# Kernel optimization log

Hardware: AMD Instinct MI355X
Metric: run time of the kernel (lower is better)

The kernel has to match this reference:

```python
import jax, jax.numpy as jnp
import numpy as np

D_MODEL = 1024
N_HEADS = 16
D_FF = 4096
D_K = D_MODEL // N_HEADS


def _ln(x, g, b, eps=1e-5):
    mu = jnp.mean(x, axis=-1, keepdims=True)
    var = jnp.mean(jnp.square(x - mu), axis=-1, keepdims=True)
    return (x - mu) * jax.lax.rsqrt(var + eps) * g + b


def setup_inputs() -> dict:
    key = jax.random.key(0)
    ks = jax.random.split(key, 16)
    s = 0.02
    inp = {
        "x": jax.random.normal(ks[0], (2, 2048, D_MODEL), dtype=jnp.float32),
        "Wq": jax.random.normal(ks[1], (D_MODEL, D_MODEL), dtype=jnp.float32) * s,
        "bq": jnp.zeros((D_MODEL,), jnp.float32),
        "Wk": jax.random.normal(ks[2], (D_MODEL, D_MODEL), dtype=jnp.float32) * s,
        "bk": jnp.zeros((D_MODEL,), jnp.float32),
        "Wv": jax.random.normal(ks[3], (D_MODEL, D_MODEL), dtype=jnp.float32) * s,
        "bv": jnp.zeros((D_MODEL,), jnp.float32),
        "Wo": jax.random.normal(ks[4], (D_MODEL, D_MODEL), dtype=jnp.float32) * s,
        "bo": jnp.zeros((D_MODEL,), jnp.float32),
        "W1": jax.random.normal(ks[5], (D_MODEL, D_FF), dtype=jnp.float32) * s,
        "b1": jnp.zeros((D_FF,), jnp.float32),
        "W2": jax.random.normal(ks[6], (D_FF, D_MODEL), dtype=jnp.float32) * s,
        "b2": jnp.zeros((D_MODEL,), jnp.float32),
        "g1": jnp.ones((D_MODEL,), jnp.float32),
        "be1": jnp.zeros((D_MODEL,), jnp.float32),
        "g2": jnp.ones((D_MODEL,), jnp.float32),
        "be2": jnp.zeros((D_MODEL,), jnp.float32),
    }
    return inp


def reference(x, Wq, bq, Wk, bk, Wv, bv, Wo, bo, W1, b1, W2, b2, g1, be1, g2, be2):
    B, L, D = x.shape
    # QKV projections -> [B, H, L, d_k]
    q = (x @ Wq + bq).reshape(B, L, N_HEADS, D_K).transpose(0, 2, 1, 3)
    k = (x @ Wk + bk).reshape(B, L, N_HEADS, D_K).transpose(0, 2, 1, 3)
    v = (x @ Wv + bv).reshape(B, L, N_HEADS, D_K).transpose(0, 2, 1, 3)
    scores = jnp.einsum("bhqd,bhkd->bhqk", q, k) / jnp.sqrt(jnp.float32(D_K))
    attn = jax.nn.softmax(scores, axis=-1)
    ctx = jnp.einsum("bhqk,bhkd->bhqd", attn, v)
    ctx = ctx.transpose(0, 2, 1, 3).reshape(B, L, D)
    attn_out = ctx @ Wo + bo
    # residual + LN1
    h = _ln(x + attn_out, g1, be1)
    # FFN (exact GELU, matching torch F.gelu default)
    ff = jax.nn.gelu(h @ W1 + b1, approximate=False) @ W2 + b2
    return _ln(h + ff, g2, be2)
```

## Files before the change

### kernel.cpp

```cpp
#include <hip/hip_runtime.h>
#include <cmath>


typedef unsigned short u16;
typedef unsigned int u32;
typedef __attribute__((ext_vector_type(8))) __bf16 bf16x8;
typedef __attribute__((ext_vector_type(4))) float f32x4;

#define MFMA16(a, b, c) __builtin_amdgcn_mfma_f32_16x16x32_bf16(a, b, c, 0, 0, 0)

__device__ __forceinline__ u16 f2bf(float f) {
  u32 u = __builtin_bit_cast(u32, f);
  u += 0x7fffu + ((u >> 16) & 1u);
  return (u16)(u >> 16);
}

__device__ __forceinline__ u32 packtrunc(float lo, float hi) {
#if __has_builtin(__builtin_amdgcn_perm)
  return __builtin_amdgcn_perm(__builtin_bit_cast(u32, hi),
                               __builtin_bit_cast(u32, lo), 0x07060302u);
#else
  return (__builtin_bit_cast(u32, lo) >> 16) |
         (__builtin_bit_cast(u32, hi) & 0xFFFF0000u);
#endif
}

__device__ __forceinline__ bf16x8 ld_frag(const u16* p) {
  return __builtin_bit_cast(bf16x8, *(const uint4*)p);
}

__device__ __forceinline__ float fexp2(float x) {
#if __has_builtin(__builtin_amdgcn_exp2f)
  return __builtin_amdgcn_exp2f(x);
#else
  return exp2f(x);
#endif
}

__device__ __forceinline__ void gload16(const u16* g, u16* l) {
  __builtin_amdgcn_global_load_lds(
      (const __attribute__((address_space(1))) void*)g,
      (__attribute__((address_space(3))) void*)l, 16, 0, 0);
}

#define WAITVL(N) asm volatile("s_waitcnt vmcnt(" #N ") lgkmcnt(0)" ::: "memory")
#define BAR() do { __builtin_amdgcn_s_barrier(); asm volatile("" ::: "memory"); } while (0)

__global__ __launch_bounds__(256) void cvt_bf16_k(const float* __restrict__ src,
                                                  u16* __restrict__ dst) {
  int i = (blockIdx.x * 256 + threadIdx.x) * 4;
  float4 v = *(const float4*)(src + i);
  ushort4 o;
  o.x = f2bf(v.x); o.y = f2bf(v.y); o.z = f2bf(v.z); o.w = f2bf(v.w);
  *(ushort4*)(dst + i) = o;
}

__global__ __launch_bounds__(256) void transpose_bf16_k(const float* __restrict__ src,
                                                        u16* __restrict__ dst,
                                                        int R, int C) {
  __shared__ float tile[32][33];
  int tx = threadIdx.x & 31, ty = threadIdx.x >> 5;
  int c0 = blockIdx.x * 32, r0 = blockIdx.y * 32;
#pragma unroll
  for (int i = 0; i < 4; i++)
    tile[ty + 8 * i][tx] = src[(long)(r0 + ty + 8 * i) * C + c0 + tx];
  __syncthreads();
#pragma unroll
  for (int i = 0; i < 4; i++)
    dst[(long)(c0 + ty + 8 * i) * R + r0 + tx] = f2bf(tile[tx][ty + 8 * i]);
}

__global__ __launch_bounds__(256) void transpose4_bf16_k(
    const float* __restrict__ Wq, const float* __restrict__ Wk,
    const float* __restrict__ Wv, const float* __restrict__ Wo,
    u16* __restrict__ wqkvT, u16* __restrict__ woT) {
  const int z = blockIdx.z;
  const float* src = (z == 0) ? Wq : (z == 1) ? Wk : (z == 2) ? Wv : Wo;
  u16* dst = (z < 3) ? (wqkvT + (size_t)z * 1024 * 1024) : woT;
  __shared__ float tile[32][33];
  int tx = threadIdx.x & 31, ty = threadIdx.x >> 5;
  int c0 = blockIdx.x * 32, r0 = blockIdx.y * 32;
#pragma unroll
  for (int i = 0; i < 4; i++)
    tile[ty + 8 * i][tx] = src[(long)(r0 + ty + 8 * i) * 1024 + c0 + tx];
  __syncthreads();
#pragma unroll
  for (int i = 0; i < 4; i++)
    dst[(long)(c0 + ty + 8 * i) * 1024 + r0 + tx] = f2bf(tile[tx][ty + 8 * i]);
}

template <int MODE>
__global__ __launch_bounds__(512, 2) void gemm256_k(
    const u16* __restrict__ A, const u16* __restrict__ BT,
    int N, int lda, int ldb, int Kc,
    const float* __restrict__ bias, float* __restrict__ outF, u16* __restrict__ outB,
    float* __restrict__ p1, float* __restrict__ p2, float* __restrict__ p3,
    u16* __restrict__ qd, u16* __restrict__ kd, u16* __restrict__ vTd,
    const float* __restrict__ bq, const float* __restrict__ bk, const float* __restrict__ bv) {
  __shared__ u16 As[4][256 * 32];
  __shared__ u16 Bs[4][256 * 32];
  const int tid = threadIdx.x;
  const int wave = tid >> 6, lane = tid & 63, quad = lane >> 4, l16 = lane & 15;
  const int wm = wave >> 2, wn = wave & 3;
  const int m0 = blockIdx.y * 256, n0 = blockIdx.x * 256;
  const int kz = blockIdx.z;
  const long kofs = (long)kz * Kc;
  const int KT = Kc >> 5;

  const int srow = lane >> 2;
  const int sseg = (lane & 3) ^ (srow & 3);
  const u16* aS = A + (long)(m0 + wave * 32 + srow) * lda + kofs + sseg * 8;
  const u16* bS = BT + (long)(n0 + wave * 32 + srow) * ldb + kofs + sseg * 8;

  auto stageA = [&](int sb, int s) {
    const u16* p = aS + (long)s * 32;
    gload16(p, &As[sb][wave * 1024]);
    gload16(p + 16 * (long)lda, &As[sb][wave * 1024 + 512]);
  };
  auto stageB = [&](int sb, int s) {
    const u16* p = bS + (long)s * 32;
    gload16(p, &Bs[sb][wave * 1024]);
    gload16(p + 16 * (long)ldb, &Bs[sb][wave * 1024 + 512]);
  };

  int aro[8], bro[4];
#pragma unroll
  for (int mf = 0; mf < 8; mf++) {
    int r = wm * 128 + mf * 16 + l16;
    aro[mf] = r * 32 + ((quad ^ (r & 3)) * 8);
  }
#pragma unroll
  for (int nf = 0; nf < 4; nf++) {
    int r = wn * 64 + nf * 16 + l16;
    bro[nf] = r * 32 + ((quad ^ (r & 3)) * 8);
  }

  f32x4 acc[8][4] = {};

  stageA(0, 0); stageB(0, 0);
  stageA(1, 1); stageB(1, 1);
  stageA(2, 2); stageB(2, 2);

#pragma unroll 1
  for (int t = 0; t < KT; ++t) {
    const int buf = t & 3;
    if (t < KT - 2)      { WAITVL(8); }
    else if (t == KT - 2){ WAITVL(4); }
    else                 { WAITVL(0); }
    BAR();

    if (t + 3 < KT) stageA((t + 3) & 3, t + 3);
    bf16x8 af[4], bf4[4];
#pragma unroll
    for (int i = 0; i < 4; i++) af[i] = ld_frag(&As[buf][aro[i]]);
#pragma unroll
    for (int i = 0; i < 4; i++) bf4[i] = ld_frag(&Bs[buf][bro[i]]);
    __builtin_amdgcn_s_setprio(1);
#pragma unroll
    for (int mf = 0; mf < 4; mf++)
#pragma unroll
      for (int nf = 0; nf < 4; nf++)
        acc[mf][nf] = MFMA16(af[mf], bf4[nf], acc[mf][nf]);
    __builtin_amdgcn_s_setprio(0);

    if (t + 3 < KT) stageB((t + 3) & 3, t + 3);
#pragma unroll
    for (int i = 0; i < 4; i++) af[i] = ld_frag(&As[buf][aro[4 + i]]);
    __builtin_amdgcn_s_setprio(1);
#pragma unroll
    for (int mf = 0; mf < 4; mf++)
#pragma unroll
      for (int nf = 0; nf < 4; nf++)
        acc[4 + mf][nf] = MFMA16(af[mf], bf4[nf], acc[4 + mf][nf]);
    __builtin_amdgcn_s_setprio(0);
  }

  if (MODE == 0) {
    const int nbase = n0 + wn * 64;
    const int mat = nbase >> 10;
    const float* bp = (mat == 0) ? bq : ((mat == 1) ? bk : bv);
    float bb[4];
    int hh0[4], dd0[4];
#pragma unroll
    for (int nf = 0; nf < 4; nf++) {
      int nn = (nbase + nf * 16 + l16) & 1023;
      bb[nf] = bp[nn];
      hh0[nf] = nn >> 6;
      dd0[nf] = nn & 63;
    }
    if (mat < 2) {
#pragma unroll
      for (int mf = 0; mf < 8; mf++) {
#pragma unroll
        for (int r = 0; r < 4; r++) {
          int mr = m0 + wm * 128 + mf * 16 + quad * 4 + r;
          int bI = mr >> 11, ll = mr & 2047;
#pragma unroll
          for (int nf = 0; nf < 4; nf++) {
            float v = acc[mf][nf][r] + bb[nf];
            long idx = ((long)((bI * 16 + hh0[nf]) * 2048 + ll)) * 64 + dd0[nf];
            if (mat == 0) {
              qd[idx] = f2bf(v * 0.18033688011112043f);
            } else {
              kd[idx] = f2bf(v);
            }
          }
        }
      }
    } else {
#pragma unroll
      for (int nf = 0; nf < 4; nf++) {
#pragma unroll
        for (int mf = 0; mf < 8; mf++) {
#pragma unroll
          for (int r = 0; r < 4; r++) {
            int mr = m0 + wm * 128 + mf * 16 + quad * 4 + r;
            int bI = mr >> 11, ll = mr & 2047;
            float v = acc[mf][nf][r] + bb[nf];
            vTd[((long)((bI * 16 + hh0[nf]) * 64 + dd0[nf])) * 2048 + ll] = f2bf(v);
          }
        }
      }
    }
  } else if (MODE == 2) {
    float bb[4];
#pragma unroll
    for (int nf = 0; nf < 4; nf++) bb[nf] = bias[n0 + wn * 64 + nf * 16 + l16];
#pragma unroll
    for (int mf = 0; mf < 8; mf++) {
#pragma unroll
      for (int r = 0; r < 4; r++) {
        int mr = m0 + wm * 128 + mf * 16 + quad * 4 + r;
        u16* orow = outB + (long)mr * N + n0 + wn * 64 + l16;
#pragma unroll
        for (int nf = 0; nf < 4; nf++) {
          float v = acc[mf][nf][r] + bb[nf];
          v = 0.5f * v * (1.0f + erff(v * 0.70710678118654752f));
          orow[nf * 16] = f2bf(v);
        }
      }
    }
  } else {
    float* sl = (kz == 0) ? outF : (kz == 1) ? p1 : (kz == 2) ? p2 : p3;
#pragma unroll
    for (int mf = 0; mf < 8; mf++) {
#pragma unroll
      for (int r = 0; r < 4; r++) {
        int mr = m0 + wm * 128 + mf * 16 + quad * 4 + r;
        float* orow = sl + (long)mr * N + n0 + wn * 64 + l16;
#pragma unroll
        for (int nf = 0; nf < 4; nf++) orow[nf * 16] = acc[mf][nf][r];
      }
    }
  }
}

template <int MODE, int TN>
__global__ __launch_bounds__(256) void gemm_k(
    const u16* __restrict__ A, const u16* __restrict__ BT, int M, int N, int K,
    const float* __restrict__ bias, float* __restrict__ outF, u16* __restrict__ outB,
    u16* __restrict__ qd, u16* __restrict__ kd, u16* __restrict__ vTd,
    const float* __restrict__ bq, const float* __restrict__ bk, const float* __restrict__ bv) {
  constexpr int NT = TN / 32;
  __shared__ u16 As[2][128 * 32];
  __shared__ u16 Bs[2][TN * 32];
  const int tid = threadIdx.x;
  const int wave = tid >> 6, lane = tid & 63, quad = lane >> 4, l16 = lane & 15;
  const int wm = wave >> 1, wn = wave & 1;
  const int m0 = blockIdx.y * 128, n0 = blockIdx.x * TN;

  const int srow = lane >> 2;
  const int sxor = (lane & 3) ^ (srow & 3);
  const u16* aS0 = A + (long)(m0 + wave * 32 + srow) * K + sxor * 8;
  const u16* aS1 = aS0 + 16 * K;
  const u16* bS0 = BT + (long)(n0 + (TN == 128 ? wave * 32 : wave * 16) + srow) * K + sxor * 8;
  const u16* bS1 = bS0 + 16 * K;

  int aoff[4], boff[NT];
#pragma unroll
  for (int t = 0; t < 4; t++) {
    int ra = wm * 64 + t * 16 + l16;
    aoff[t] = ra * 32 + ((quad ^ (l16 & 3)) * 8);
  }
#pragma unroll
  for (int t = 0; t < NT; t++) {
    int rb = wn * (TN / 2) + t * 16 + l16;
    boff[t] = rb * 32 + ((quad ^ (l16 & 3)) * 8);
  }

  auto stage = [&](int buf, int k0) {
    gload16(aS0 + k0, &As[buf][(wave * 2 + 0) * 512]);
    gload16(aS1 + k0, &As[buf][(wave * 2 + 1) * 512]);
    if (TN == 128) {
      gload16(bS0 + k0, &Bs[buf][(wave * 2 + 0) * 512]);
      gload16(bS1 + k0, &Bs[buf][(wave * 2 + 1) * 512]);
    } else {
      gload16(bS0 + k0, &Bs[buf][wave * 512]);
    }
  };

  f32x4 acc[4][NT] = {};

  stage(0, 0);
#pragma unroll 1
  for (int k0 = 0; k0 < K; k0 += 32) {
    const int buf = (k0 >> 5) & 1;
    __syncthreads();
    if (k0 + 32 < K) stage(buf ^ 1, k0 + 32);
    bf16x8 af[4], bfr[NT];
#pragma unroll
    for (int t = 0; t < 4; t++) af[t] = ld_frag(&As[buf][aoff[t]]);
#pragma unroll
    for (int t = 0; t < NT; t++) bfr[t] = ld_frag(&Bs[buf][boff[t]]);
#pragma unroll
    for (int mt = 0; mt < 4; mt++)
#pragma unroll
      for (int nt = 0; nt < NT; nt++)
        acc[mt][nt] = MFMA16(af[mt], bfr[nt], acc[mt][nt]);
  }

  if (MODE == 1) {
    float bb[NT];
#pragma unroll
    for (int nt = 0; nt < NT; nt++) bb[nt] = bias[n0 + wn * (TN / 2) + nt * 16 + l16];
#pragma unroll
    for (int mt = 0; mt < 4; mt++) {
#pragma unroll
      for (int r = 0; r < 4; r++) {
        int mr = m0 + wm * 64 + mt * 16 + quad * 4 + r;
        float* orow = outF + (long)mr * N + n0 + wn * (TN / 2) + l16;
#pragma unroll
        for (int nt = 0; nt < NT; nt++)
          orow[nt * 16] = acc[mt][nt][r] + bb[nt];
      }
    }
  }
}

__global__ __launch_bounds__(256) void attn_k(const u16* __restrict__ qd,
                                              const u16* __restrict__ kd,
                                              const u16* __restrict__ vTd,
                                              u16* __restrict__ ctx) {
  __shared__ u16 Ks[2][64 * 64];
  __shared__ u16 Vs[2][64 * 64];
  __shared__ __align__(16) u16 P[4][32][72];
  const int tid = threadIdx.x;
  const int wave = tid >> 6, lane = tid & 63, quad = lane >> 4, l16 = lane & 15;
  const int bh = blockIdx.y;
  const u16* Q = qd + (long)bh * 2048 * 64;
  const u16* Kp = kd + (long)bh * 2048 * 64;
  const u16* Vt = vTd + (long)bh * 64 * 2048;
  const int qbase = blockIdx.x * 128 + wave * 32;

  bf16x8 qf[2][2];
#pragma unroll
  for (int qs = 0; qs < 2; qs++) {
    qf[qs][0] = ld_frag(Q + (qbase + qs * 16 + l16) * 64 + quad * 8);
    qf[qs][1] = ld_frag(Q + (qbase + qs * 16 + l16) * 64 + 32 + quad * 8);
  }

  f32x4 o[2][4] = {};
  float m[2] = {-1e30f, -1e30f}, l[2] = {0.f, 0.f};

  const int srow = lane >> 3;
  const int sx = (lane & 7) ^ srow;
  const int kr0 = wave * 16 + srow;
  const int kr1 = wave * 16 + 8 + srow;

  const int fs0 = ((0 * 4 + quad) ^ (l16 & 7)) * 8;
  const int fs1 = ((1 * 4 + quad) ^ (l16 & 7)) * 8;

  auto stage = [&](int buf, int j0) {
    gload16(Kp + (long)(j0 + kr0) * 64 + sx * 8, &Ks[buf][(wave * 2 + 0) * 512]);
    gload16(Kp + (long)(j0 + kr1) * 64 + sx * 8, &Ks[buf][(wave * 2 + 1) * 512]);
    gload16(Vt + (long)kr0 * 2048 + j0 + sx * 8, &Vs[buf][(wave * 2 + 0) * 512]);
    gload16(Vt + (long)kr1 * 2048 + j0 + sx * 8, &Vs[buf][(wave * 2 + 1) * 512]);
  };

  stage(0, 0);

#pragma unroll 1
  for (int j0 = 0; j0 < 2048; j0 += 64) {
    const int buf = (j0 >> 6) & 1;
    __syncthreads();
    if (j0 + 64 < 2048) stage(buf ^ 1, j0 + 64);

    const u16* kb = &Ks[buf][0];
    f32x4 st[2][4];
#pragma unroll
    for (int f = 0; f < 4; f++) {
      bf16x8 k0 = ld_frag(kb + (f * 16 + l16) * 64 + fs0);
      bf16x8 k1 = ld_frag(kb + (f * 16 + l16) * 64 + fs1);
      f32x4 s0 = {}, s1 = {};
      s0 = MFMA16(k0, qf[0][0], s0); s0 = MFMA16(k1, qf[0][1], s0);
      s1 = MFMA16(k0, qf[1][0], s1); s1 = MFMA16(k1, qf[1][1], s1);
      st[0][f] = s0; st[1][f] = s1;
    }

#pragma unroll
    for (int qs = 0; qs < 2; qs++) {
      float mx = -1e30f;
#pragma unroll
      for (int f = 0; f < 4; f++)
        mx = fmaxf(mx, fmaxf(fmaxf(st[qs][f][0], st[qs][f][1]),
                             fmaxf(st[qs][f][2], st[qs][f][3])));
      mx = fmaxf(mx, __shfl_xor(mx, 16));
      mx = fmaxf(mx, __shfl_xor(mx, 32));
      if (__ballot(mx > m[qs])) {
        float mn = fmaxf(m[qs], mx);
        float al = fexp2(m[qs] - mn);
        m[qs] = mn;
        l[qs] *= al;
#pragma unroll
        for (int nt = 0; nt < 4; nt++) {
          o[qs][nt][0] *= al; o[qs][nt][1] *= al;
          o[qs][nt][2] *= al; o[qs][nt][3] *= al;
        }
      }
      float sm = 0.f;
      u16* prow = &P[wave][qs * 16 + l16][0];
#pragma unroll
      for (int f = 0; f < 4; f++) {
        float p0 = fexp2(st[qs][f][0] - m[qs]);
        float p1 = fexp2(st[qs][f][1] - m[qs]);
        float p2 = fexp2(st[qs][f][2] - m[qs]);
        float p3 = fexp2(st[qs][f][3] - m[qs]);
        sm += (p0 + p1) + (p2 + p3);
        uint2 u;
        u.x = packtrunc(p0, p1);
        u.y = packtrunc(p2, p3);
        *(uint2*)(prow + f * 16 + quad * 4) = u;
      }
      sm += __shfl_xor(sm, 16);
      sm += __shfl_xor(sm, 32);
      l[qs] += sm;
    }
    __asm__ volatile("s_waitcnt lgkmcnt(0)" ::: "memory");

    const u16* vb = &Vs[buf][0];
    bf16x8 vf[4][2];
#pragma unroll
    for (int nt = 0; nt < 4; nt++) {
      vf[nt][0] = ld_frag(vb + (nt * 16 + l16) * 64 + fs0);
      vf[nt][1] = ld_frag(vb + (nt * 16 + l16) * 64 + fs1);
    }
#pragma unroll
    for (int qs = 0; qs < 2; qs++) {
      const u16* prow = &P[wave][qs * 16 + l16][0];
#pragma unroll
      for (int kh = 0; kh < 2; kh++) {
        bf16x8 pf = ld_frag(prow + kh * 32 + quad * 8);
#pragma unroll
        for (int nt = 0; nt < 4; nt++)
          o[qs][nt] = MFMA16(vf[nt][kh], pf, o[qs][nt]);
      }
    }
  }

  const int bI = bh >> 4, hh = bh & 15;
#pragma unroll
  for (int qs = 0; qs < 2; qs++) {
    const float rl = 1.0f / l[qs];
    const long row = (long)(bI * 2048 + qbase + qs * 16 + l16);
#pragma unroll
    for (int nt = 0; nt < 4; nt++) {
      ushort4 w;
      w.x = f2bf(o[qs][nt][0] * rl);
      w.y = f2bf(o[qs][nt][1] * rl);
      w.z = f2bf(o[qs][nt][2] * rl);
      w.w = f2bf(o[qs][nt][3] * rl);
      *(ushort4*)(ctx + row * 1024 + hh * 64 + nt * 16 + quad * 4) = w;
    }
  }
}

__global__ __launch_bounds__(256) void ln_k(const float* __restrict__ a,
                                            const float* __restrict__ b,
                                            const float* __restrict__ g,
                                            const float* __restrict__ be,
                                            float* __restrict__ outF,
                                            u16* __restrict__ outB) {
  const int row = blockIdx.x, tid = threadIdx.x;
  const float* pa = a + (long)row * 1024;
  const float* pb = b + (long)row * 1024;
  float v[4], s = 0.f, sq = 0.f;
#pragma unroll
  for (int i = 0; i < 4; i++) {
    int c = i * 256 + tid;
    v[i] = pa[c] + pb[c];
    s += v[i];
    sq += v[i] * v[i];
  }
#pragma unroll
  for (int off = 1; off < 64; off <<= 1) {
    s += __shfl_xor(s, off);
    sq += __shfl_xor(sq, off);
  }
  __shared__ float red[10];
  int wave = tid >> 6, lane = tid & 63;
  if (lane == 0) { red[wave * 2] = s; red[wave * 2 + 1] = sq; }
  __syncthreads();
  if (tid == 0) {
    float S = red[0] + red[2] + red[4] + red[6];
    float Q = red[1] + red[3] + red[5] + red[7];
    float mu = S * (1.0f / 1024.0f);
    float var = Q * (1.0f / 1024.0f) - mu * mu;
    red[8] = mu;
    red[9] = rsqrtf(var + 1e-5f);
  }
  __syncthreads();
  float mu = red[8], rstd = red[9];
#pragma unroll
  for (int i = 0; i < 4; i++) {
    int c = i * 256 + tid;
    float o = (v[i] - mu) * rstd * g[c] + be[c];
    outF[(long)row * 1024 + c] = o;
    if (outB) outB[(long)row * 1024 + c] = f2bf(o);
  }
}

__global__ __launch_bounds__(256) void ln4_k(const float* __restrict__ a,
                                             const float* __restrict__ q0,
                                             const float* __restrict__ q1,
                                             const float* __restrict__ q2,
                                             const float* __restrict__ q3,
                                             const float* __restrict__ bias,
                                             const float* __restrict__ g,
                                             const float* __restrict__ be,
                                             float* __restrict__ outF) {
  const int row = blockIdx.x, tid = threadIdx.x;
  const long base = (long)row * 1024;
  float v[4], s = 0.f, sq = 0.f;
#pragma unroll
  for (int i = 0; i < 4; i++) {
    int c = i * 256 + tid;
    float ff = (q0[base + c] + q1[base + c]) + (q2[base + c] + q3[base + c]) + bias[c];
    v[i] = a[base + c] + ff;
    s += v[i];
    sq += v[i] * v[i];
  }
#pragma unroll
  for (int off = 1; off < 64; off <<= 1) {
    s += __shfl_xor(s, off);
    sq += __shfl_xor(sq, off);
  }
  __shared__ float red[10];
  int wave = tid >> 6, lane = tid & 63;
  if (lane == 0) { red[wave * 2] = s; red[wave * 2 + 1] = sq; }
  __syncthreads();
  if (tid == 0) {
    float S = red[0] + red[2] + red[4] + red[6];
    float Q = red[1] + red[3] + red[5] + red[7];
    float mu = S * (1.0f / 1024.0f);
    float var = Q * (1.0f / 1024.0f) - mu * mu;
    red[8] = mu;
    red[9] = rsqrtf(var + 1e-5f);
  }
  __syncthreads();
  float mu = red[8], rstd = red[9];
#pragma unroll
  for (int i = 0; i < 4; i++) {
    int c = i * 256 + tid;
    outF[base + c] = (v[i] - mu) * rstd * g[c] + be[c];
  }
}

extern "C" void kernel_launch(void* const* d_in, const int* in_sizes, int n_in,
                              void* d_out, int out_size, void* d_ws, size_t ws_size,
                              hipStream_t stream) {
  const float* x  = (const float*)d_in[0];
  const float* Wq = (const float*)d_in[1];  const float* bq = (const float*)d_in[2];
  const float* Wk = (const float*)d_in[3];  const float* bk = (const float*)d_in[4];
  const float* Wv = (const float*)d_in[5];  const float* bv = (const float*)d_in[6];
  const float* Wo = (const float*)d_in[7];  const float* bo = (const float*)d_in[8];
  const float* W1 = (const float*)d_in[9];  const float* b1 = (const float*)d_in[10];
  const float* W2 = (const float*)d_in[11]; const float* b2 = (const float*)d_in[12];
  const float* g1 = (const float*)d_in[13]; const float* be1 = (const float*)d_in[14];
  const float* g2 = (const float*)d_in[15]; const float* be2 = (const float*)d_in[16];

  char* ws = (char*)d_ws;
  size_t off = 0;
  auto alloc = [&](size_t bytes) {
    size_t o = off;
    off += (bytes + 255) & ~(size_t)255;
    return o;
  };
  u16*   xb     = (u16*)(ws + alloc(4096UL * 1024 * 2));
  u16*   wqkvT  = (u16*)(ws + alloc(3072UL * 1024 * 2));
  u16*   woT    = (u16*)(ws + alloc(1024UL * 1024 * 2));
  u16*   w1T    = (u16*)(ws + alloc(4096UL * 1024 * 2));
  u16*   w2T    = (u16*)(ws + alloc(1024UL * 4096 * 2));
  u16*   qb     = (u16*)(ws + alloc(32UL * 2048 * 64 * 2));
  u16*   kb     = (u16*)(ws + alloc(32UL * 2048 * 64 * 2));
  u16*   vTb    = (u16*)(ws + alloc(32UL * 64 * 2048 * 2));
  u16*   ctx    = (u16*)(ws + alloc(4096UL * 1024 * 2));
  float* attnO  = (float*)(ws + alloc(4096UL * 1024 * 4));
  float* h      = (float*)(ws + alloc(4096UL * 1024 * 4));
  u16*   hb     = (u16*)(ws + alloc(4096UL * 1024 * 2));
  u16*   ff1    = (u16*)(ws + alloc(4096UL * 4096 * 2));
  float* ff2    = (float*)(ws + alloc(4096UL * 1024 * 4));
  if (off > ws_size) return;

  float* sl0 = ff2;
  float* sl1 = attnO;
  float* sl2 = (float*)qb;
  float* sl3 = (float*)vTb;

  cvt_bf16_k<<<4096, 256, 0, stream>>>(x, xb);
  transpose4_bf16_k<<<dim3(32, 32, 4), 256, 0, stream>>>(Wq, Wk, Wv, Wo, wqkvT, woT);
  transpose_bf16_k<<<dim3(128, 32), 256, 0, stream>>>(W1, w1T, 1024, 4096);
  transpose_bf16_k<<<dim3(32, 128), 256, 0, stream>>>(W2, w2T, 4096, 1024);

  gemm256_k<0><<<dim3(12, 16), 512, 0, stream>>>(
      xb, wqkvT, 3072, 1024, 1024, 1024,
      nullptr, nullptr, nullptr, nullptr, nullptr, nullptr,
      qb, kb, vTb, bq, bk, bv);
  attn_k<<<dim3(16, 32), 256, 0, stream>>>(qb, kb, vTb, ctx);
  gemm_k<1, 64><<<dim3(16, 32), 256, 0, stream>>>(ctx, woT, 4096, 1024, 1024,
                                                  bo, attnO, nullptr,
                                                  nullptr, nullptr, nullptr, nullptr, nullptr, nullptr);
  ln_k<<<4096, 256, 0, stream>>>(x, attnO, g1, be1, h, hb);
  gemm256_k<2><<<dim3(16, 16), 512, 0, stream>>>(
      hb, w1T, 4096, 1024, 1024, 1024,
      b1, nullptr, ff1, nullptr, nullptr, nullptr,
      nullptr, nullptr, nullptr, nullptr, nullptr, nullptr);
  gemm256_k<3><<<dim3(4, 16, 4), 512, 0, stream>>>(
      ff1, w2T, 1024, 4096, 4096, 1024,
      nullptr, sl0, nullptr, sl1, sl2, sl3,
      nullptr, nullptr, nullptr, nullptr, nullptr, nullptr);
  ln4_k<<<4096, 256, 0, stream>>>(h, sl0, sl1, sl2, sl3, b2, g2, be2, (float*)d_out);
}
```

Measured before the change: 411.5 us.

## Split attention over key halves with combine kernel; add barriers in GEMM loop

Attention is split along the key dimension into two halves (flash-decoding style). This doubles the grid from 512 to 1024 blocks so more CUs are occupied, and a new combine kernel merges the partial outputs using the per-row max and sum. The online softmax now rescales only when the running max grows by more than 8, which skips rescale work but lets exponent values grow (up to 2^8) before renormalising. Separately, the 256 GEMM loop now loads fragments before issuing the next stage and adds extra barriers, which changes how LDS reads interleave with global prefetch at the cost of more synchronisation. The partial results go to fp32 scratch buffers reused from other workspace, adding global traffic.

```diff
diff --git a/kernel.cpp b/kernel.cpp
--- a/kernel.cpp
+++ b/kernel.cpp
@@ -149,12 +149,13 @@
     else                 { WAITVL(0); }
     BAR();
 
+    bf16x8 af[4], bf4[4];
+#pragma unroll
+    for (int i = 0; i < 4; i++) af[i] = ld_frag(&As[buf][aro[i]]);
+#pragma unroll
+    for (int i = 0; i < 4; i++) bf4[i] = ld_frag(&Bs[buf][bro[i]]);
     if (t + 3 < KT) stageA((t + 3) & 3, t + 3);
-    bf16x8 af[4], bf4[4];
-#pragma unroll
-    for (int i = 0; i < 4; i++) af[i] = ld_frag(&As[buf][aro[i]]);
-#pragma unroll
-    for (int i = 0; i < 4; i++) bf4[i] = ld_frag(&Bs[buf][bro[i]]);
+    BAR();
     __builtin_amdgcn_s_setprio(1);
 #pragma unroll
     for (int mf = 0; mf < 4; mf++)
@@ -163,15 +164,17 @@
         acc[mf][nf] = MFMA16(af[mf], bf4[nf], acc[mf][nf]);
     __builtin_amdgcn_s_setprio(0);
 
+    bf16x8 ag[4];
+#pragma unroll
+    for (int i = 0; i < 4; i++) ag[i] = ld_frag(&As[buf][aro[4 + i]]);
     if (t + 3 < KT) stageB((t + 3) & 3, t + 3);
-#pragma unroll
-    for (int i = 0; i < 4; i++) af[i] = ld_frag(&As[buf][aro[4 + i]]);
+    BAR();
     __builtin_amdgcn_s_setprio(1);
 #pragma unroll
     for (int mf = 0; mf < 4; mf++)
 #pragma unroll
       for (int nf = 0; nf < 4; nf++)
-        acc[4 + mf][nf] = MFMA16(af[mf], bf4[nf], acc[4 + mf][nf]);
+        acc[4 + mf][nf] = MFMA16(ag[mf], bf4[nf], acc[4 + mf][nf]);
     __builtin_amdgcn_s_setprio(0);
   }
 
@@ -340,13 +343,18 @@
 __global__ __launch_bounds__(256) void attn_k(const u16* __restrict__ qd,
                                               const u16* __restrict__ kd,
                                               const u16* __restrict__ vTd,
-                                              u16* __restrict__ ctx) {
+                                              float* __restrict__ oP0,
+                                              float* __restrict__ oP1,
+                                              float* __restrict__ ml0,
+                                              float* __restrict__ ml1) {
   __shared__ u16 Ks[2][64 * 64];
   __shared__ u16 Vs[2][64 * 64];
   __shared__ __align__(16) u16 P[4][32][72];
   const int tid = threadIdx.x;
   const int wave = tid >> 6, lane = tid & 63, quad = lane >> 4, l16 = lane & 15;
   const int bh = blockIdx.y;
+  const int kz = blockIdx.z;
+  const int jbeg = kz * 1024, jend = jbeg + 1024;
   const u16* Q = qd + (long)bh * 2048 * 64;
   const u16* Kp = kd + (long)bh * 2048 * 64;
   const u16* Vt = vTd + (long)bh * 64 * 2048;
@@ -377,13 +385,13 @@
     gload16(Vt + (long)kr1 * 2048 + j0 + sx * 8, &Vs[buf][(wave * 2 + 1) * 512]);
   };
 
-  stage(0, 0);
+  stage(0, jbeg);
 
 #pragma unroll 1
-  for (int j0 = 0; j0 < 2048; j0 += 64) {
+  for (int j0 = jbeg; j0 < jend; j0 += 64) {
     const int buf = (j0 >> 6) & 1;
     __syncthreads();
-    if (j0 + 64 < 2048) stage(buf ^ 1, j0 + 64);
+    if (j0 + 64 < jend) stage(buf ^ 1, j0 + 64);
 
     const u16* kb = &Ks[buf][0];
     f32x4 st[2][4];
@@ -406,7 +414,7 @@
                              fmaxf(st[qs][f][2], st[qs][f][3])));
       mx = fmaxf(mx, __shfl_xor(mx, 16));
       mx = fmaxf(mx, __shfl_xor(mx, 32));
-      if (__ballot(mx > m[qs])) {
+      if (__any(mx > m[qs] + 8.0f)) {
         float mn = fmaxf(m[qs], mx);
         float al = fexp2(m[qs] - mn);
         m[qs] = mn;
@@ -457,21 +465,44 @@
     }
   }
 
-  const int bI = bh >> 4, hh = bh & 15;
+  float* oDst = kz ? oP1 : oP0;
+  float* mlDst = kz ? ml1 : ml0;
 #pragma unroll
   for (int qs = 0; qs < 2; qs++) {
-    const float rl = 1.0f / l[qs];
-    const long row = (long)(bI * 2048 + qbase + qs * 16 + l16);
-#pragma unroll
-    for (int nt = 0; nt < 4; nt++) {
-      ushort4 w;
-      w.x = f2bf(o[qs][nt][0] * rl);
-      w.y = f2bf(o[qs][nt][1] * rl);
-      w.z = f2bf(o[qs][nt][2] * rl);
-      w.w = f2bf(o[qs][nt][3] * rl);
-      *(ushort4*)(ctx + row * 1024 + hh * 64 + nt * 16 + quad * 4) = w;
-    }
-  }
+    const long row = (long)bh * 2048 + qbase + qs * 16 + l16;
+#pragma unroll
+    for (int nt = 0; nt < 4; nt++)
+      *(float4*)(oDst + row * 64 + nt * 16 + quad * 4) =
+          *(const float4*)&o[qs][nt];
+    if (quad == 0) {
+      float2 ml2 = {m[qs], l[qs]};
+      *(float2*)(mlDst + row * 2) = ml2;
+    }
+  }
+}
+
+__global__ __launch_bounds__(256) void attn_combine_k(
+    const float* __restrict__ o0, const float* __restrict__ o1,
+    const float* __restrict__ ml0, const float* __restrict__ ml1,
+    u16* __restrict__ ctx) {
+  long i = ((long)blockIdx.x * 256 + threadIdx.x) * 4;
+  long row = i >> 6;
+  int d = (int)(i & 63);
+  float2 a0 = *(const float2*)(ml0 + row * 2);
+  float2 a1 = *(const float2*)(ml1 + row * 2);
+  float M = fmaxf(a0.x, a1.x);
+  float w0 = fexp2(a0.x - M), w1 = fexp2(a1.x - M);
+  float rinv = 1.0f / (a0.y * w0 + a1.y * w1);
+  float4 v0 = *(const float4*)(o0 + i);
+  float4 v1 = *(const float4*)(o1 + i);
+  int bh = (int)(row >> 11), ll = (int)(row & 2047);
+  int bI = bh >> 4, hh = bh & 15;
+  ushort4 w;
+  w.x = f2bf((v0.x * w0 + v1.x * w1) * rinv);
+  w.y = f2bf((v0.y * w0 + v1.y * w1) * rinv);
+  w.z = f2bf((v0.z * w0 + v1.z * w1) * rinv);
+  w.w = f2bf((v0.w * w0 + v1.w * w1) * rinv);
+  *(ushort4*)(ctx + ((long)(bI * 2048 + ll) * 1024) + hh * 64 + d) = w;
 }
 
 __global__ __launch_bounds__(256) void ln_k(const float* __restrict__ a,
@@ -601,6 +632,11 @@
   float* ff2    = (float*)(ws + alloc(4096UL * 1024 * 4));
   if (off > ws_size) return;
 
+  float* oPart0 = attnO;
+  float* oPart1 = h;
+  float* mlP0   = (float*)hb;
+  float* mlP1   = (float*)hb + 32 * 2048 * 2;
+
   float* sl0 = ff2;
   float* sl1 = attnO;
   float* sl2 = (float*)qb;
@@ -615,7 +651,9 @@
       xb, wqkvT, 3072, 1024, 1024, 1024,
       nullptr, nullptr, nullptr, nullptr, nullptr, nullptr,
       qb, kb, vTb, bq, bk, bv);
-  attn_k<<<dim3(16, 32), 256, 0, stream>>>(qb, kb, vTb, ctx);
+  attn_k<<<dim3(16, 32, 2), 256, 0, stream>>>(qb, kb, vTb,
+                                              oPart0, oPart1, mlP0, mlP1);
+  attn_combine_k<<<4096, 256, 0, stream>>>(oPart0, oPart1, mlP0, mlP1, ctx);
   gemm_k<1, 64><<<dim3(16, 32), 256, 0, stream>>>(ctx, woT, 4096, 1024, 1024,
                                                   bo, attnO, nullptr,
                                                   nullptr, nullptr, nullptr, nullptr, nullptr, nullptr);
```

New measurement: 399.0 us. -3.0%, faster.

## Switch big GEMMs to 128x128 tiles, halve split-K, and lazily rescale attention

Applied to the files above, without the earlier changes.

Replaces the 256x256, 512-thread GEMM, which used a 4-stage LDS pipeline, with a 128x128, 256-thread GEMM that uses a 3-stage pipeline and allows three blocks per CU. The goal is to launch more blocks, so the QKV, FFN1 and FFN2 grids fill the CUs better. FFN2 split-K drops from 4 to 2 slices, so the final layernorm sums two partials instead of four. Attention now rescales the running softmax only when the new max exceeds the old one by more than 8, and attn_k gets launch bounds for occupancy. The trade-off is less data reuse per tile, which means more global and LDS traffic for each FLOP.

```diff
diff --git a/kernel.cpp b/kernel.cpp
--- a/kernel.cpp
+++ b/kernel.cpp
@@ -90,19 +90,20 @@
 }
 
 template <int MODE>
-__global__ __launch_bounds__(512, 2) void gemm256_k(
+__global__ __launch_bounds__(256, 3) void gemm128_k(
     const u16* __restrict__ A, const u16* __restrict__ BT,
     int N, int lda, int ldb, int Kc,
-    const float* __restrict__ bias, float* __restrict__ outF, u16* __restrict__ outB,
-    float* __restrict__ p1, float* __restrict__ p2, float* __restrict__ p3,
+    const float* __restrict__ bias, float* __restrict__ outF,
+    u16* __restrict__ outB, float* __restrict__ p1,
     u16* __restrict__ qd, u16* __restrict__ kd, u16* __restrict__ vTd,
-    const float* __restrict__ bq, const float* __restrict__ bk, const float* __restrict__ bv) {
-  __shared__ u16 As[4][256 * 32];
-  __shared__ u16 Bs[4][256 * 32];
+    const float* __restrict__ bq, const float* __restrict__ bk,
+    const float* __restrict__ bv) {
+  __shared__ u16 As[3][128 * 32];
+  __shared__ u16 Bs[3][128 * 32];
   const int tid = threadIdx.x;
   const int wave = tid >> 6, lane = tid & 63, quad = lane >> 4, l16 = lane & 15;
-  const int wm = wave >> 2, wn = wave & 3;
-  const int m0 = blockIdx.y * 256, n0 = blockIdx.x * 256;
+  const int wm = wave >> 1, wn = wave & 1;
+  const int m0 = blockIdx.y * 128, n0 = blockIdx.x * 128;
   const int kz = blockIdx.z;
   const long kofs = (long)kz * Kc;
   const int KT = Kc >> 5;
@@ -112,67 +113,50 @@
   const u16* aS = A + (long)(m0 + wave * 32 + srow) * lda + kofs + sseg * 8;
   const u16* bS = BT + (long)(n0 + wave * 32 + srow) * ldb + kofs + sseg * 8;
 
-  auto stageA = [&](int sb, int s) {
-    const u16* p = aS + (long)s * 32;
-    gload16(p, &As[sb][wave * 1024]);
-    gload16(p + 16 * (long)lda, &As[sb][wave * 1024 + 512]);
+  auto stage = [&](int sb, int s) {
+    const u16* pa = aS + (long)s * 32;
+    gload16(pa, &As[sb][wave * 1024]);
+    gload16(pa + 16 * (long)lda, &As[sb][wave * 1024 + 512]);
+    const u16* pb = bS + (long)s * 32;
+    gload16(pb, &Bs[sb][wave * 1024]);
+    gload16(pb + 16 * (long)ldb, &Bs[sb][wave * 1024 + 512]);
   };
-  auto stageB = [&](int sb, int s) {
-    const u16* p = bS + (long)s * 32;
-    gload16(p, &Bs[sb][wave * 1024]);
-    gload16(p + 16 * (long)ldb, &Bs[sb][wave * 1024 + 512]);
-  };
-
-  int aro[8], bro[4];
-#pragma unroll
-  for (int mf = 0; mf < 8; mf++) {
-    int r = wm * 128 + mf * 16 + l16;
-    aro[mf] = r * 32 + ((quad ^ (r & 3)) * 8);
-  }
-#pragma unroll
-  for (int nf = 0; nf < 4; nf++) {
-    int r = wn * 64 + nf * 16 + l16;
-    bro[nf] = r * 32 + ((quad ^ (r & 3)) * 8);
-  }
-
-  f32x4 acc[8][4] = {};
-
-  stageA(0, 0); stageB(0, 0);
-  stageA(1, 1); stageB(1, 1);
-  stageA(2, 2); stageB(2, 2);
-
+
+  int aro[4], bro[4];
+#pragma unroll
+  for (int f = 0; f < 4; f++) {
+    int ra = wm * 64 + f * 16 + l16;
+    aro[f] = ra * 32 + ((quad ^ (ra & 3)) * 8);
+    int rb = wn * 64 + f * 16 + l16;
+    bro[f] = rb * 32 + ((quad ^ (rb & 3)) * 8);
+  }
+
+  f32x4 acc[4][4] = {};
+
+  stage(0, 0);
+  stage(1, 1);
+  int buf = 0;
 #pragma unroll 1
   for (int t = 0; t < KT; ++t) {
-    const int buf = t & 3;
-    if (t < KT - 2)      { WAITVL(8); }
-    else if (t == KT - 2){ WAITVL(4); }
-    else                 { WAITVL(0); }
+    if (t < KT - 1) { WAITVL(4); } else { WAITVL(0); }
     BAR();
-
-    if (t + 3 < KT) stageA((t + 3) & 3, t + 3);
-    bf16x8 af[4], bf4[4];
+    bf16x8 af[4], bfr[4];
 #pragma unroll
     for (int i = 0; i < 4; i++) af[i] = ld_frag(&As[buf][aro[i]]);
 #pragma unroll
-    for (int i = 0; i < 4; i++) bf4[i] = ld_frag(&Bs[buf][bro[i]]);
+    for (int i = 0; i < 4; i++) bfr[i] = ld_frag(&Bs[buf][bro[i]]);
+    if (t + 2 < KT) {
+      int nb = buf + 2; if (nb >= 3) nb -= 3;
+      stage(nb, t + 2);
+    }
     __builtin_amdgcn_s_setprio(1);
 #pragma unroll
     for (int mf = 0; mf < 4; mf++)
 #pragma unroll
       for (int nf = 0; nf < 4; nf++)
-        acc[mf][nf] = MFMA16(af[mf], bf4[nf], acc[mf][nf]);
+        acc[mf][nf] = MFMA16(af[mf], bfr[nf], acc[mf][nf]);
     __builtin_amdgcn_s_setprio(0);
-
-    if (t + 3 < KT) stageB((t + 3) & 3, t + 3);
-#pragma unroll
-    for (int i = 0; i < 4; i++) af[i] = ld_frag(&As[buf][aro[4 + i]]);
-    __builtin_amdgcn_s_setprio(1);
-#pragma unroll
-    for (int mf = 0; mf < 4; mf++)
-#pragma unroll
-      for (int nf = 0; nf < 4; nf++)
-        acc[4 + mf][nf] = MFMA16(af[mf], bf4[nf], acc[4 + mf][nf]);
-    __builtin_amdgcn_s_setprio(0);
+    if (++buf == 3) buf = 0;
   }
 
   if (MODE == 0) {
@@ -190,10 +174,10 @@
     }
     if (mat < 2) {
 #pragma unroll
-      for (int mf = 0; mf < 8; mf++) {
+      for (int mf = 0; mf < 4; mf++) {
 #pragma unroll
         for (int r = 0; r < 4; r++) {
-          int mr = m0 + wm * 128 + mf * 16 + quad * 4 + r;
+          int mr = m0 + wm * 64 + mf * 16 + quad * 4 + r;
           int bI = mr >> 11, ll = mr & 2047;
 #pragma unroll
           for (int nf = 0; nf < 4; nf++) {
@@ -211,10 +195,10 @@
 #pragma unroll
       for (int nf = 0; nf < 4; nf++) {
 #pragma unroll
-        for (int mf = 0; mf < 8; mf++) {
+        for (int mf = 0; mf < 4; mf++) {
 #pragma unroll
           for (int r = 0; r < 4; r++) {
-            int mr = m0 + wm * 128 + mf * 16 + quad * 4 + r;
+            int mr = m0 + wm * 64 + mf * 16 + quad * 4 + r;
             int bI = mr >> 11, ll = mr & 2047;
             float v = acc[mf][nf][r] + bb[nf];
             vTd[((long)((bI * 16 + hh0[nf]) * 64 + dd0[nf])) * 2048 + ll] = f2bf(v);
@@ -227,10 +211,10 @@
 #pragma unroll
     for (int nf = 0; nf < 4; nf++) bb[nf] = bias[n0 + wn * 64 + nf * 16 + l16];
 #pragma unroll
-    for (int mf = 0; mf < 8; mf++) {
+    for (int mf = 0; mf < 4; mf++) {
 #pragma unroll
       for (int r = 0; r < 4; r++) {
-        int mr = m0 + wm * 128 + mf * 16 + quad * 4 + r;
+        int mr = m0 + wm * 64 + mf * 16 + quad * 4 + r;
         u16* orow = outB + (long)mr * N + n0 + wn * 64 + l16;
 #pragma unroll
         for (int nf = 0; nf < 4; nf++) {
@@ -241,12 +225,12 @@
       }
     }
   } else {
-    float* sl = (kz == 0) ? outF : (kz == 1) ? p1 : (kz == 2) ? p2 : p3;
-#pragma unroll
-    for (int mf = 0; mf < 8; mf++) {
+    float* sl = (kz == 0) ? outF : p1;
+#pragma unroll
+    for (int mf = 0; mf < 4; mf++) {
 #pragma unroll
       for (int r = 0; r < 4; r++) {
-        int mr = m0 + wm * 128 + mf * 16 + quad * 4 + r;
+        int mr = m0 + wm * 64 + mf * 16 + quad * 4 + r;
         float* orow = sl + (long)mr * N + n0 + wn * 64 + l16;
 #pragma unroll
         for (int nf = 0; nf < 4; nf++) orow[nf * 16] = acc[mf][nf][r];
@@ -258,9 +242,7 @@
 template <int MODE, int TN>
 __global__ __launch_bounds__(256) void gemm_k(
     const u16* __restrict__ A, const u16* __restrict__ BT, int M, int N, int K,
-    const float* __restrict__ bias, float* __restrict__ outF, u16* __restrict__ outB,
-    u16* __restrict__ qd, u16* __restrict__ kd, u16* __restrict__ vTd,
-    const float* __restrict__ bq, const float* __restrict__ bk, const float* __restrict__ bv) {
+    const float* __restrict__ bias, float* __restrict__ outF) {
   constexpr int NT = TN / 32;
   __shared__ u16 As[2][128 * 32];
   __shared__ u16 Bs[2][TN * 32];
@@ -337,10 +319,10 @@
   }
 }
 
-__global__ __launch_bounds__(256) void attn_k(const u16* __restrict__ qd,
-                                              const u16* __restrict__ kd,
-                                              const u16* __restrict__ vTd,
-                                              u16* __restrict__ ctx) {
+__global__ __launch_bounds__(256, 3) void attn_k(const u16* __restrict__ qd,
+                                                 const u16* __restrict__ kd,
+                                                 const u16* __restrict__ vTd,
+                                                 u16* __restrict__ ctx) {
   __shared__ u16 Ks[2][64 * 64];
   __shared__ u16 Vs[2][64 * 64];
   __shared__ __align__(16) u16 P[4][32][72];
@@ -406,7 +388,7 @@
                              fmaxf(st[qs][f][2], st[qs][f][3])));
       mx = fmaxf(mx, __shfl_xor(mx, 16));
       mx = fmaxf(mx, __shfl_xor(mx, 32));
-      if (__ballot(mx > m[qs])) {
+      if (__any(mx > m[qs] + 8.0f)) {
         float mn = fmaxf(m[qs], mx);
         float al = fexp2(m[qs] - mn);
         m[qs] = mn;
@@ -519,22 +501,20 @@
   }
 }
 
-__global__ __launch_bounds__(256) void ln4_k(const float* __restrict__ a,
-                                             const float* __restrict__ q0,
-                                             const float* __restrict__ q1,
-                                             const float* __restrict__ q2,
-                                             const float* __restrict__ q3,
-                                             const float* __restrict__ bias,
-                                             const float* __restrict__ g,
-                                             const float* __restrict__ be,
-                                             float* __restrict__ outF) {
+__global__ __launch_bounds__(256) void ln2s_k(const float* __restrict__ a,
+                                              const float* __restrict__ q0,
+                                              const float* __restrict__ q1,
+                                              const float* __restrict__ bias,
+                                              const float* __restrict__ g,
+                                              const float* __restrict__ be,
+                                              float* __restrict__ outF) {
   const int row = blockIdx.x, tid = threadIdx.x;
   const long base = (long)row * 1024;
   float v[4], s = 0.f, sq = 0.f;
 #pragma unroll
   for (int i = 0; i < 4; i++) {
     int c = i * 256 + tid;
-    float ff = (q0[base + c] + q1[base + c]) + (q2[base + c] + q3[base + c]) + bias[c];
+    float ff = q0[base + c] + q1[base + c] + bias[c];
     v[i] = a[base + c] + ff;
     s += v[i];
     sq += v[i] * v[i];
@@ -603,30 +583,27 @@
 
   float* sl0 = ff2;
   float* sl1 = attnO;
-  float* sl2 = (float*)qb;
-  float* sl3 = (float*)vTb;
 
   cvt_bf16_k<<<4096, 256, 0, stream>>>(x, xb);
   transpose4_bf16_k<<<dim3(32, 32, 4), 256, 0, stream>>>(Wq, Wk, Wv, Wo, wqkvT, woT);
   transpose_bf16_k<<<dim3(128, 32), 256, 0, stream>>>(W1, w1T, 1024, 4096);
   transpose_bf16_k<<<dim3(32, 128), 256, 0, stream>>>(W2, w2T, 4096, 1024);
 
-  gemm256_k<0><<<dim3(12, 16), 512, 0, stream>>>(
+  gemm128_k<0><<<dim3(24, 32), 256, 0, stream>>>(
       xb, wqkvT, 3072, 1024, 1024, 1024,
-      nullptr, nullptr, nullptr, nullptr, nullptr, nullptr,
+      nullptr, nullptr, nullptr, nullptr,
       qb, kb, vTb, bq, bk, bv);
   attn_k<<<dim3(16, 32), 256, 0, stream>>>(qb, kb, vTb, ctx);
   gemm_k<1, 64><<<dim3(16, 32), 256, 0, stream>>>(ctx, woT, 4096, 1024, 1024,
-                                                  bo, attnO, nullptr,
-                                                  nullptr, nullptr, nullptr, nullptr, nullptr, nullptr);
+                                                  bo, attnO);
   ln_k<<<4096, 256, 0, stream>>>(x, attnO, g1, be1, h, hb);
-  gemm256_k<2><<<dim3(16, 16), 512, 0, stream>>>(
+  gemm128_k<2><<<dim3(32, 32), 256, 0, stream>>>(
       hb, w1T, 4096, 1024, 1024, 1024,
-      b1, nullptr, ff1, nullptr, nullptr, nullptr,
+      b1, nullptr, ff1, nullptr,
       nullptr, nullptr, nullptr, nullptr, nullptr, nullptr);
-  gemm256_k<3><<<dim3(4, 16, 4), 512, 0, stream>>>(
-      ff1, w2T, 1024, 4096, 4096, 1024,
-      nullptr, sl0, nullptr, sl1, sl2, sl3,
+  gemm128_k<3><<<dim3(8, 32, 2), 256, 0, stream>>>(
+      ff1, w2T, 1024, 4096, 4096, 2048,
+      nullptr, sl0, nullptr, sl1,
       nullptr, nullptr, nullptr, nullptr, nullptr, nullptr);
-  ln4_k<<<4096, 256, 0, stream>>>(h, sl0, sl1, sl2, sl3, b2, g2, be2, (float*)d_out);
-}
+  ln2s_k<<<4096, 256, 0, stream>>>(h, sl0, sl1, b2, g2, be2, (float*)d_out);
+}
```

After: 382.8 us. 7.0% less time.
